# Optimization experiments

Measured on AMD Instinct MI355X. Metric: run time of the kernel, lower is better.

Reference implementation:

```python
import jax, jax.numpy as jnp
import numpy as np

NUM_EXPERTS = 8
HIDDEN = 2048
EXPERT_DIM = 2048  # intermediate_size per shard (tp_size=1)
TOTAL_TOKENS = 32768  # divisible by NUM_EXPERTS


def setup_inputs() -> dict:
    key = jax.random.key(0)
    k1, k2, k3 = jax.random.split(key, 3)
    hidden_states = jax.random.normal(k1, (TOTAL_TOKENS, HIDDEN), dtype=jnp.float32)
    # (E, H, 2*D): gate and up projections concatenated on last dim
    gate_up_proj = jax.random.normal(k2, (NUM_EXPERTS, HIDDEN, 2 * EXPERT_DIM), dtype=jnp.float32) * 0.02
    # (E, D, H)
    down_proj = jax.random.normal(k3, (NUM_EXPERTS, EXPERT_DIM, HIDDEN), dtype=jnp.float32) * 0.02
    return {"hidden_states": hidden_states, "gate_up_proj": gate_up_proj, "down_proj": down_proj}


def reference(hidden_states, gate_up_proj, down_proj):
    E, H = gate_up_proj.shape[0], gate_up_proj.shape[1]
    # tokens are pre-sorted per expert: (E, T, H)
    x = hidden_states.reshape(E, -1, H)
    # grouped GEMM: (E,T,H) @ (E,H,2D) -> (E,T,2D)
    gate_up = jnp.einsum('eth,ehd->etd', x, gate_up_proj)
    gate, up = jnp.split(gate_up, 2, axis=-1)
    # SwiGLU epilogue then down projection: (E,T,D) @ (E,D,H) -> (E,T,H)
    act = up * jax.nn.silu(gate)
    out = jnp.einsum('etd,edh->eth', act, down_proj)
    # tp_size=1 -> all_reduce is identity
    return out.reshape(-1, H)
```

## Files before the change

kernel.cpp:

```cpp
#include <hip/hip_runtime.h>


#define E_EXPERTS 8
#define TPE 4096
#define KD 2048

typedef __bf16 bf16_t;
typedef __bf16 bf16x4 __attribute__((ext_vector_type(4)));
typedef __bf16 bf16x8 __attribute__((ext_vector_type(8)));
typedef float f32x4 __attribute__((ext_vector_type(4)));

#define GLOAD16(src, dst)                                               \
  __builtin_amdgcn_global_load_lds(                                     \
      (const __attribute__((address_space(1))) void*)(src),             \
      (__attribute__((address_space(3))) void*)(dst), 16, 0, 0)

__global__ void cvt_f32_bf16_kernel(const float* __restrict__ in,
                                    bf16_t* __restrict__ out, long n4) {
  long i = (long)blockIdx.x * blockDim.x + threadIdx.x;
  const long stride = (long)gridDim.x * blockDim.x;
  const float4* in4 = (const float4*)in;
  bf16x4* out4 = (bf16x4*)out;
  for (; i < n4; i += stride) {
    float4 v = in4[i];
    bf16x4 o = {(bf16_t)v.x, (bf16_t)v.y, (bf16_t)v.z, (bf16_t)v.w};
    out4[i] = o;
  }
}

__global__ void transpose_cvt_kernel(const float* __restrict__ W,
                                     bf16_t* __restrict__ WT, int K, int N) {
  __shared__ float tile[64][65];
  const int e = blockIdx.z;
  const float* Wp = W + (size_t)e * K * N;
  bf16_t* Tp = WT + (size_t)e * N * K;
  const int n0 = blockIdx.x * 64, k0 = blockIdx.y * 64;
  const int rr = threadIdx.x >> 4;
  const int cc = (threadIdx.x & 15) * 4;
#pragma unroll
  for (int p = 0; p < 4; ++p) {
    const int k = rr + p * 16;
    float4 v = *(const float4*)(Wp + (size_t)(k0 + k) * N + n0 + cc);
    tile[k][cc + 0] = v.x;
    tile[k][cc + 1] = v.y;
    tile[k][cc + 2] = v.z;
    tile[k][cc + 3] = v.w;
  }
  __syncthreads();
#pragma unroll
  for (int p = 0; p < 4; ++p) {
    const int n = rr + p * 16;
    bf16x4 o;
#pragma unroll
    for (int j = 0; j < 4; ++j) o[j] = (bf16_t)tile[cc + j][n];
    *(bf16x4*)(Tp + (size_t)(n0 + n) * K + k0 + cc) = o;
  }
}

#define MMA_QUAD(QM, QN, BF)                                                 \
  do {                                                                       \
    _Pragma("unroll") for (int kk = 0; kk < 2; ++kk) {                       \
      _Pragma("unroll") for (int m = 0; m < 4; ++m) {                        \
        _Pragma("unroll") for (int n = 0; n < 2; ++n) {                      \
          acc[(QM)*4 + m][(QN)*2 + n] =                                      \
              __builtin_amdgcn_mfma_f32_16x16x32_bf16(                       \
                  af[m][kk], BF[n][kk], acc[(QM)*4 + m][(QN)*2 + n], 0, 0, 0); \
        }                                                                    \
      }                                                                      \
    }                                                                        \
  } while (0)

template <bool FUSED, int NTN>
__global__ __launch_bounds__(512, 2) void moe_gemm8_kernel(
    const bf16_t* __restrict__ A, const bf16_t* __restrict__ Bm,
    void* __restrict__ Cout) {
  constexpr int NT = KD / 64;
  constexpr int NWG = E_EXPERTS * 16 * NTN;

  __shared__ alignas(16) bf16_t As[2][256][64];
  __shared__ alignas(16) bf16_t Bs[2][256][64];

  int wg = blockIdx.x;
  wg = (wg & 7) * (NWG / 8) + (wg >> 3);
  const int e = wg / (16 * NTN);
  const int rem = wg % (16 * NTN);
  const int mt = rem / NTN, ntile = rem % NTN;
  const int t0 = mt * 256, n0 = ntile * 256;

  const int tid = threadIdx.x;
  const int wid = tid >> 6, lane = tid & 63;
  const int wr = wid >> 2, wc = wid & 3;

  const bf16_t* Ae = A + (size_t)e * TPE * KD + (size_t)t0 * KD;
  const bf16_t* Be = Bm + (size_t)e * (size_t)(FUSED ? 4096 : 2048) * KD;

  const int slr = lane >> 3;
  const int sel = ((lane & 7) ^ slr) * 8;

  auto stageA = [&](int kt, int h) {
    const int ktw = kt & (NT - 1);
    const int k0 = ktw * 64;
    const int buf = kt & 1;
#pragma unroll
    for (int i = 0; i < 2; ++i) {
      const int r0 = h * 128 + wid * 16 + i * 8;
      GLOAD16(Ae + (size_t)(r0 + slr) * KD + k0 + sel, &As[buf][r0][0]);
    }
  };
  auto stageB = [&](int kt, int h) {
    const int ktw = kt & (NT - 1);
    const int k0 = ktw * 64;
    const int buf = kt & 1;
#pragma unroll
    for (int i = 0; i < 2; ++i) {
      const int r0 = h * 128 + wid * 16 + i * 8;
      const int R = n0 + r0 + slr;
      int srow;
      if constexpr (FUSED)
        srow = ((R >> 5) << 4) + (R & 15) + ((R >> 4) & 1) * 2048;
      else
        srow = R;
      GLOAD16(Be + (size_t)srow * KD + k0 + sel, &Bs[buf][r0][0]);
    }
  };

  const int la = lane & 15, kg4 = lane >> 4;

  f32x4 acc[8][4] = {};
  bf16x8 af[4][2];
  bf16x8 b0[2][2];
  bf16x8 b1[2][2];

  auto readA = [&](int buf, int qm) {
#pragma unroll
    for (int m = 0; m < 4; ++m) {
      const int row = wr * 128 + qm * 64 + m * 16 + la;
#pragma unroll
      for (int kk = 0; kk < 2; ++kk) {
        const int ch = ((kk * 4 + kg4) ^ (la & 7)) * 8;
        af[m][kk] = *(const bf16x8*)&As[buf][row][ch];
      }
    }
  };
  auto readB = [&](int buf, int qn, bf16x8 (&bf)[2][2]) {
#pragma unroll
    for (int n = 0; n < 2; ++n) {
      const int row = wc * 64 + qn * 32 + n * 16 + la;
#pragma unroll
      for (int kk = 0; kk < 2; ++kk) {
        const int ch = ((kk * 4 + kg4) ^ (la & 7)) * 8;
        bf[n][kk] = *(const bf16x8*)&Bs[buf][row][ch];
      }
    }
  };

#define LGKM0 asm volatile("s_waitcnt lgkmcnt(0)" ::: "memory")
#define VMC4 asm volatile("s_waitcnt vmcnt(4)" ::: "memory")
#define BAR __builtin_amdgcn_s_barrier()
#define SCHED0 __builtin_amdgcn_sched_barrier(0)
#define PRIO1 __builtin_amdgcn_s_setprio(1)
#define PRIO0 __builtin_amdgcn_s_setprio(0)

  stageA(0, 0); stageA(0, 1);
  stageB(0, 0); stageB(0, 1);
  stageB(1, 0); stageB(1, 1);
  VMC4;
  BAR;
  readB(0, 0, b0);

  auto tile = [&](int kt, int buf) {
    readA(buf, 0);
    stageA(kt + 1, 0);
    BAR; LGKM0; SCHED0;
    PRIO1; MMA_QUAD(0, 0, b0); PRIO0;
    BAR;
    readB(buf, 1, b1);
    stageA(kt + 1, 1);
    BAR; LGKM0; SCHED0;
    PRIO1; MMA_QUAD(0, 1, b1); PRIO0;
    BAR;
    readA(buf, 1);
    stageB(kt + 2, 0);
    BAR; LGKM0; SCHED0;
    PRIO1; MMA_QUAD(1, 1, b1); PRIO0;
    BAR;
    stageB(kt + 2, 1);
    PRIO1; MMA_QUAD(1, 0, b0); PRIO0;
    VMC4;
    readB(buf ^ 1, 0, b0);
    BAR;
  };

  for (int kt = 0; kt < NT; kt += 2) {
    tile(kt, 0);
    tile(kt + 1, 1);
  }

  const int lg = lane >> 4;
  const int rbase = t0 + wr * 128;
  if constexpr (FUSED) {
    bf16_t* Cp = (bf16_t*)Cout + (size_t)e * TPE * KD;
    const int jb = (n0 + wc * 64) >> 1;
#pragma unroll
    for (int m = 0; m < 8; ++m)
#pragma unroll
      for (int p = 0; p < 2; ++p)
#pragma unroll
        for (int r = 0; r < 4; ++r) {
          const int row = rbase + m * 16 + lg * 4 + r;
          const int col = jb + p * 16 + la;
          const float g = acc[m][2 * p][r], u = acc[m][2 * p + 1][r];
          const float s = 1.0f / (1.0f + __expf(-g));
          Cp[(size_t)row * KD + col] = (bf16_t)(u * g * s);
        }
  } else {
    float* Cp = (float*)Cout + (size_t)e * TPE * KD;
#pragma unroll
    for (int m = 0; m < 8; ++m)
#pragma unroll
      for (int n = 0; n < 4; ++n)
#pragma unroll
        for (int r = 0; r < 4; ++r) {
          const int row = rbase + m * 16 + lg * 4 + r;
          const int col = n0 + wc * 64 + n * 16 + la;
          Cp[(size_t)row * KD + col] = acc[m][n][r];
        }
  }
#undef LGKM0
#undef VMC4
#undef BAR
#undef SCHED0
#undef PRIO1
#undef PRIO0
}

extern "C" void kernel_launch(void* const* d_in, const int* in_sizes, int n_in,
                              void* d_out, int out_size, void* d_ws,
                              size_t ws_size, hipStream_t stream) {
  const float* hs = (const float*)d_in[0];
  const float* w1 = (const float*)d_in[1];
  const float* w2 = (const float*)d_in[2];

  char* ws = (char*)d_ws;
  bf16_t* xb = (bf16_t*)(ws);
  bf16_t* w1t = (bf16_t*)(ws + (size_t)134217728);
  bf16_t* w2t = (bf16_t*)(ws + (size_t)268435456);
  bf16_t* act = (bf16_t*)(ws + (size_t)335544320);

  const long n4 = (long)E_EXPERTS * TPE * KD / 4;
  cvt_f32_bf16_kernel<<<2048, 256, 0, stream>>>(hs, xb, n4);
  transpose_cvt_kernel<<<dim3(64, 32, 8), 256, 0, stream>>>(w1, w1t, 2048, 4096);
  transpose_cvt_kernel<<<dim3(32, 32, 8), 256, 0, stream>>>(w2, w2t, 2048, 2048);
  moe_gemm8_kernel<true, 16><<<2048, 512, 0, stream>>>(xb, w1t, (void*)act);
  moe_gemm8_kernel<false, 8><<<1024, 512, 0, stream>>>(act, w2t, d_out);
}
```

Measured before the change: 1.177 ms.

## Restructure GEMM main loop into finer-grained A-fragment pipeline with partial LDS waits

Splits the per-tile MFMA work into eight 2x2 chunks using ping-pong A-fragment registers (afP/afQ) and alternating B fragment buffers. Replaces full lgkmcnt(0) waits with partial lgkmcnt(8)/(4) waits and removes several barriers so LDS reads overlap MFMA issue more tightly. It also reads the workgroup count from gridDim instead of a compile-time constant. Correctness depends on the partial wait counts matching the order in which LDS reads are issued, and the extra fragment buffers raise register pressure.

```diff
diff --git a/kernel.cpp b/kernel.cpp
--- a/kernel.cpp
+++ b/kernel.cpp
@@ -57,14 +57,15 @@
   }
 }
 
-#define MMA_QUAD(QM, QN, BF)                                                 \
+#define MMA_H(MP, AF, BF, QN)                                                \
   do {                                                                       \
     _Pragma("unroll") for (int kk = 0; kk < 2; ++kk) {                       \
-      _Pragma("unroll") for (int m = 0; m < 4; ++m) {                        \
+      _Pragma("unroll") for (int mm = 0; mm < 2; ++mm) {                     \
         _Pragma("unroll") for (int n = 0; n < 2; ++n) {                      \
-          acc[(QM)*4 + m][(QN)*2 + n] =                                      \
+          acc[(MP)*2 + mm][(QN)*2 + n] =                                     \
               __builtin_amdgcn_mfma_f32_16x16x32_bf16(                       \
-                  af[m][kk], BF[n][kk], acc[(QM)*4 + m][(QN)*2 + n], 0, 0, 0); \
+                  AF[mm][kk], BF[n][kk], acc[(MP)*2 + mm][(QN)*2 + n], 0, 0, \
+                  0);                                                        \
         }                                                                    \
       }                                                                      \
     }                                                                        \
@@ -75,13 +76,13 @@
     const bf16_t* __restrict__ A, const bf16_t* __restrict__ Bm,
     void* __restrict__ Cout) {
   constexpr int NT = KD / 64;
-  constexpr int NWG = E_EXPERTS * 16 * NTN;
 
   __shared__ alignas(16) bf16_t As[2][256][64];
   __shared__ alignas(16) bf16_t Bs[2][256][64];
 
+  const int NWG = gridDim.x;
   int wg = blockIdx.x;
-  wg = (wg & 7) * (NWG / 8) + (wg >> 3);
+  wg = (wg & 7) * (NWG >> 3) + (wg >> 3);
   const int e = wg / (16 * NTN);
   const int rem = wg % (16 * NTN);
   const int mt = rem / NTN, ntile = rem % NTN;
@@ -127,73 +128,92 @@
   const int la = lane & 15, kg4 = lane >> 4;
 
   f32x4 acc[8][4] = {};
-  bf16x8 af[4][2];
-  bf16x8 b0[2][2];
-  bf16x8 b1[2][2];
-
-  auto readA = [&](int buf, int qm) {
-#pragma unroll
-    for (int m = 0; m < 4; ++m) {
-      const int row = wr * 128 + qm * 64 + m * 16 + la;
+  bf16x8 afP[2][2], afQ[2][2];
+  bf16x8 bA[2][2], bB[2][2];
+
+  auto readAh = [&](int buf, int mp, bf16x8 (&dst)[2][2]) {
+#pragma unroll
+    for (int mm = 0; mm < 2; ++mm) {
+      const int row = wr * 128 + mp * 32 + mm * 16 + la;
 #pragma unroll
       for (int kk = 0; kk < 2; ++kk) {
         const int ch = ((kk * 4 + kg4) ^ (la & 7)) * 8;
-        af[m][kk] = *(const bf16x8*)&As[buf][row][ch];
+        dst[mm][kk] = *(const bf16x8*)&As[buf][row][ch];
       }
     }
   };
-  auto readB = [&](int buf, int qn, bf16x8 (&bf)[2][2]) {
+  auto readBh = [&](int buf, int qn, bf16x8 (&dst)[2][2]) {
 #pragma unroll
     for (int n = 0; n < 2; ++n) {
       const int row = wc * 64 + qn * 32 + n * 16 + la;
 #pragma unroll
       for (int kk = 0; kk < 2; ++kk) {
         const int ch = ((kk * 4 + kg4) ^ (la & 7)) * 8;
-        bf[n][kk] = *(const bf16x8*)&Bs[buf][row][ch];
+        dst[n][kk] = *(const bf16x8*)&Bs[buf][row][ch];
       }
     }
   };
 
-#define LGKM0 asm volatile("s_waitcnt lgkmcnt(0)" ::: "memory")
+#define W8 asm volatile("s_waitcnt lgkmcnt(8)" ::: "memory")
+#define W4 asm volatile("s_waitcnt lgkmcnt(4)" ::: "memory")
+#define W0 asm volatile("s_waitcnt lgkmcnt(0)" ::: "memory")
 #define VMC4 asm volatile("s_waitcnt vmcnt(4)" ::: "memory")
 #define BAR __builtin_amdgcn_s_barrier()
 #define SCHED0 __builtin_amdgcn_sched_barrier(0)
 #define PRIO1 __builtin_amdgcn_s_setprio(1)
 #define PRIO0 __builtin_amdgcn_s_setprio(0)
 
+#define TILE(kt, buf, BX, BY)                          \
+  do {                                                 \
+                                               \
+    readBh(buf, 1, BY);                                \
+    readAh(buf, 1, afQ);                               \
+    stageA((kt) + 1, 0);                               \
+    W8; SCHED0;                                        \
+    PRIO1; MMA_H(0, afP, BX, 0); PRIO0;                \
+                                               \
+    W4; SCHED0;                                        \
+    PRIO1; MMA_H(0, afP, BY, 1); PRIO0;                \
+    BAR;                                               \
+                                               \
+    readAh(buf, 2, afP);                               \
+    stageA((kt) + 1, 1);                               \
+    W4; SCHED0;                                        \
+    PRIO1; MMA_H(1, afQ, BY, 1); PRIO0;                \
+                                               \
+    PRIO1; MMA_H(1, afQ, BX, 0); PRIO0;                \
+    BAR;                                               \
+                                               \
+    readAh(buf, 3, afQ);                               \
+    stageB((kt) + 2, 0);                               \
+    W4; SCHED0;                                        \
+    PRIO1; MMA_H(2, afP, BX, 0); PRIO0;                \
+                                               \
+    PRIO1; MMA_H(2, afP, BY, 1); PRIO0;                \
+    BAR;                                               \
+                                               \
+    stageB((kt) + 2, 1);                               \
+    W0; SCHED0;                                        \
+    PRIO1; MMA_H(3, afQ, BY, 1); PRIO0;                \
+                                               \
+    VMC4;                                              \
+    readAh((buf) ^ 1, 0, afP);                         \
+    readBh((buf) ^ 1, 0, BY);                          \
+    PRIO1; MMA_H(3, afQ, BX, 0); PRIO0;                \
+    BAR;                                               \
+  } while (0)
+
   stageA(0, 0); stageA(0, 1);
   stageB(0, 0); stageB(0, 1);
   stageB(1, 0); stageB(1, 1);
   VMC4;
   BAR;
-  readB(0, 0, b0);
-
-  auto tile = [&](int kt, int buf) {
-    readA(buf, 0);
-    stageA(kt + 1, 0);
-    BAR; LGKM0; SCHED0;
-    PRIO1; MMA_QUAD(0, 0, b0); PRIO0;
-    BAR;
-    readB(buf, 1, b1);
-    stageA(kt + 1, 1);
-    BAR; LGKM0; SCHED0;
-    PRIO1; MMA_QUAD(0, 1, b1); PRIO0;
-    BAR;
-    readA(buf, 1);
-    stageB(kt + 2, 0);
-    BAR; LGKM0; SCHED0;
-    PRIO1; MMA_QUAD(1, 1, b1); PRIO0;
-    BAR;
-    stageB(kt + 2, 1);
-    PRIO1; MMA_QUAD(1, 0, b0); PRIO0;
-    VMC4;
-    readB(buf ^ 1, 0, b0);
-    BAR;
-  };
+  readAh(0, 0, afP);
+  readBh(0, 0, bA);
 
   for (int kt = 0; kt < NT; kt += 2) {
-    tile(kt, 0);
-    tile(kt + 1, 1);
+    TILE(kt, 0, bA, bB);
+    TILE(kt + 1, 1, bB, bA);
   }
 
   const int lg = lane >> 4;
@@ -226,7 +246,9 @@
           Cp[(size_t)row * KD + col] = acc[m][n][r];
         }
   }
-#undef LGKM0
+#undef W8
+#undef W4
+#undef W0
 #undef VMC4
 #undef BAR
 #undef SCHED0
```

New measurement: 1.115 ms. 5.3% less time.
